# Kernel tuning notes

Hardware: AMD Instinct MI355X
Metric: run time of the kernel (lower is better)

Reference implementation:

```python
import jax, jax.numpy as jnp
import numpy as np

N = 384        # n_res
C = 128        # c_pair
H = 4          # num_head
DH = C // H    # qkv_dim = 32
LN_EPS = 1e-5
NEG_INF = -1e9


def setup_inputs() -> dict:
    key = jax.random.key(0)
    ks = jax.random.split(key, 8)
    s = 0.02
    return {
        "pair": jax.random.normal(ks[0], (N, N, C), dtype=jnp.float32),
        "mask": jax.random.randint(ks[1], (N, N), 0, 2, dtype=jnp.int32),
        "ln_w": jnp.ones((C,), dtype=jnp.float32),
        "ln_b": jnp.zeros((C,), dtype=jnp.float32),
        "w_bias": jax.random.normal(ks[2], (C, H), dtype=jnp.float32) * s,
        "wq": jax.random.normal(ks[3], (C, C), dtype=jnp.float32) * s,
        "wk": jax.random.normal(ks[4], (C, C), dtype=jnp.float32) * s,
        "wv": jax.random.normal(ks[5], (C, C), dtype=jnp.float32) * s,
        "wg": jax.random.normal(ks[6], (C, C), dtype=jnp.float32) * s,
        "wo": jax.random.normal(ks[7], (C, C), dtype=jnp.float32) * s,
    }


def reference(pair, mask, ln_w, ln_b, w_bias, wq, wk, wv, wg, wo):
    # LayerNorm over c_pair (biased variance, as torch)
    mu = pair.mean(-1, keepdims=True)
    var = jnp.mean(jnp.square(pair - mu), axis=-1, keepdims=True)
    x = (pair - mu) * jax.lax.rsqrt(var + LN_EPS) * ln_w + ln_b  # [N,N,C]

    # per-head pair bias: [H, N, N] (query axis q, key axis k)
    bias = jnp.einsum('qkc,ch->hqk', x, w_bias)

    # QKV + gating projections (no bias)
    q = jnp.einsum('bkc,cd->bkd', x, wq).reshape(N, N, H, DH)
    k = jnp.einsum('bkc,cd->bkd', x, wk).reshape(N, N, H, DH)
    v = jnp.einsum('bkc,cd->bkd', x, wv).reshape(N, N, H, DH)

    scale = 1.0 / np.sqrt(DH).astype(np.float32)
    logits = jnp.einsum('bqhd,bkhd->bhqk', q, k) * scale + bias[None]  # [N,H,N,N]
    # mask[b, k]: disallow attending to masked keys in row b
    logits = jnp.where(mask[:, None, None, :] > 0, logits, NEG_INF)
    probs = jax.nn.softmax(logits, axis=-1)

    o = jnp.einsum('bhqk,bkhd->bqhd', probs, v).reshape(N, N, C)
    gate = jax.nn.sigmoid(jnp.einsum('bqc,cd->bqd', x, wg))
    out = jnp.einsum('bqc,cd->bqd', o * gate, wo)  # [N,N,C]
    return out
```

## Files before the change

kernel.cpp:

```cpp
#include <hip/hip_runtime.h>
#include <hip/hip_bf16.h>
#include <stdint.h>

#define NRES 384
#define CPAIR 128
#define NHEAD 4
#define DHEAD 32
#define MROWS (NRES * NRES)
#define QK_SCALE 0.17677669529663687f
#define LOG2E 1.4426950408889634f
#define QK_L2E (0.17677669529663687f * 1.4426950408889634f)

typedef unsigned short u16;
typedef short bf16x8 __attribute__((ext_vector_type(8)));
typedef float f32x4 __attribute__((ext_vector_type(4)));

__device__ __forceinline__ u16 f2bf(float f) {
  union { float f; uint32_t u; } c; c.f = f;
  uint32_t u = c.u + 0x7fff + ((c.u >> 16) & 1);
  return (u16)(u >> 16);
}
__device__ __forceinline__ float bf2f(u16 h) {
  union { uint32_t u; float f; } c; c.u = ((uint32_t)h) << 16; return c.f;
}
__device__ __forceinline__ float fast_exp2(float x) {
#if __has_builtin(__builtin_amdgcn_exp2f)
  return __builtin_amdgcn_exp2f(x);
#else
  return exp2f(x);
#endif
}
__device__ __forceinline__ uint32_t cvt_pk_bf16(float lo, float hi) {
  uint32_t r;
  asm("v_cvt_pk_bf16_f32 %0, %1, %2" : "=v"(r) : "v"(lo), "v"(hi));
  return r;
}

__global__ void prep_kernel(const float* __restrict__ wq, const float* __restrict__ wk,
                            const float* __restrict__ wv, const float* __restrict__ wg,
                            const float* __restrict__ wb, const float* __restrict__ wo,
                            u16* __restrict__ wcat, u16* __restrict__ wot) {
  int tid = blockIdx.x * blockDim.x + threadIdx.x;
  int stride = gridDim.x * blockDim.x;
  for (int i = tid; i < 576 * 128; i += stride) {
    int n = i >> 7, kk = i & 127;
    float val;
    if (n < 128)      val = wq[kk * 128 + n] * QK_L2E;
    else if (n < 256) val = wk[kk * 128 + (n - 128)];
    else if (n < 384) val = wv[kk * 128 + (n - 256)];
    else if (n < 512) val = wg[kk * 128 + (n - 384)];
    else if (n < 516) val = wb[kk * 4 + (n - 512)] * LOG2E;
    else              val = 0.f;
    wcat[i] = f2bf(val);
  }
  for (int i = tid; i < 128 * 128; i += stride) {
    int n = i >> 7, kk = i & 127;
    wot[i] = f2bf(wo[kk * 128 + n]);
  }
}

__global__ __launch_bounds__(256) void proj_kernel(
    const float* __restrict__ pair, const float* __restrict__ lnw,
    const float* __restrict__ lnb, const u16* __restrict__ wcat,
    u16* __restrict__ q, u16* __restrict__ k, u16* __restrict__ v,
    u16* __restrict__ g, float* __restrict__ biasL) {
  __shared__ __align__(16) u16 xs[64 * 136];
  __shared__ __align__(16) u16 wsm[64 * 136];
  const int m0 = blockIdx.x * 64;
  const int tid = threadIdx.x;
  {
    const int row = tid >> 2, q4 = tid & 3;
    const float* pr = pair + (size_t)(m0 + row) * CPAIR + q4 * 32;
    float4 vals[8];
    float s1 = 0.f, s2 = 0.f;
#pragma unroll
    for (int i = 0; i < 8; ++i) {
      vals[i] = ((const float4*)pr)[i];
      s1 += (vals[i].x + vals[i].y) + (vals[i].z + vals[i].w);
      s2 += vals[i].x * vals[i].x + vals[i].y * vals[i].y +
            vals[i].z * vals[i].z + vals[i].w * vals[i].w;
    }
    s1 += __shfl_xor(s1, 1); s1 += __shfl_xor(s1, 2);
    s2 += __shfl_xor(s2, 1); s2 += __shfl_xor(s2, 2);
    const float mu = s1 * (1.f / 128.f);
    const float rs = rsqrtf(s2 * (1.f / 128.f) - mu * mu + 1e-5f);
    const float* wr = lnw + q4 * 32;
    const float* br = lnb + q4 * 32;
    uint32_t packed[16];
#pragma unroll
    for (int i = 0; i < 8; ++i) {
      float4 w4 = ((const float4*)wr)[i];
      float4 b4 = ((const float4*)br)[i];
      float y0 = (vals[i].x - mu) * rs * w4.x + b4.x;
      float y1 = (vals[i].y - mu) * rs * w4.y + b4.y;
      float y2 = (vals[i].z - mu) * rs * w4.z + b4.z;
      float y3 = (vals[i].w - mu) * rs * w4.w + b4.w;
      packed[i * 2]     = (uint32_t)f2bf(y0) | ((uint32_t)f2bf(y1) << 16);
      packed[i * 2 + 1] = (uint32_t)f2bf(y2) | ((uint32_t)f2bf(y3) << 16);
    }
#pragma unroll
    for (int i = 0; i < 4; ++i)
      *(uint4*)&xs[row * 136 + q4 * 32 + i * 8] = *(uint4*)&packed[i * 4];
  }
  const int w = tid >> 6, lane = tid & 63, lm = lane & 15, quad = lane >> 4;
  const int srow = tid >> 4, scol8 = (tid & 15) * 8;

  {
    uint4 st[4];
#pragma unroll
    for (int i = 0; i < 4; ++i)
      st[i] = *(const uint4*)&wcat[(size_t)(srow + i * 16) * CPAIR + scol8];
#pragma unroll
    for (int i = 0; i < 4; ++i)
      *(uint4*)&wsm[(srow + i * 16) * 136 + scol8] = st[i];
  }
  __syncthreads();

  for (int nc = 0; nc < 9; ++nc) {
    if (nc > 0) __syncthreads();
    f32x4 acc[4] = {{0, 0, 0, 0}, {0, 0, 0, 0}, {0, 0, 0, 0}, {0, 0, 0, 0}};
#pragma unroll
    for (int ks = 0; ks < 4; ++ks) {
      bf16x8 a = *(const bf16x8*)&xs[(w * 16 + lm) * 136 + ks * 32 + quad * 8];
#pragma unroll
      for (int nt = 0; nt < 4; ++nt) {
        if (nc == 8 && nt > 0) continue;
        bf16x8 bb = *(const bf16x8*)&wsm[(nt * 16 + lm) * 136 + ks * 32 + quad * 8];
        acc[nt] = __builtin_amdgcn_mfma_f32_16x16x32_bf16(a, bb, acc[nt], 0, 0, 0);
      }
    }
    __syncthreads();
    const bool pf = (nc + 1) < 9;
    uint4 st[4];
    if (pf) {
#pragma unroll
      for (int i = 0; i < 4; ++i) {
        if ((nc + 1) == 8 && i > 0) break;
        st[i] = *(const uint4*)&wcat[(size_t)((nc + 1) * 64 + srow + i * 16) * CPAIR + scol8];
      }
    }
#pragma unroll
    for (int nt = 0; nt < 4; ++nt) {
      if (nc == 8 && nt > 0) continue;
      int n = nc * 64 + nt * 16 + lm;
#pragma unroll
      for (int r = 0; r < 4; ++r) {
        size_t m = (size_t)(m0 + w * 16 + quad * 4 + r);
        float val = acc[nt][r];
        if (n < 128)      q[m * CPAIR + n] = f2bf(val);
        else if (n < 256) k[m * CPAIR + (n - 128)] = f2bf(val);
        else if (n < 384) v[m * CPAIR + (n - 256)] = f2bf(val);
        else if (n < 512) g[m * CPAIR + (n - 384)] = f2bf(1.f / (1.f + __expf(-val)));
        else if (n < 516) {
          int h = n - 512;
          int q_idx = (int)(m / NRES), k_idx = (int)(m % NRES);
          int qt = q_idx >> 6, l6 = q_idx & 63;
          int ww = l6 >> 4, lmq = l6 & 15;
          int t = k_idx >> 4, qk = (k_idx >> 2) & 3, rk = k_idx & 3;
          size_t idx = ((size_t)((h * 6 + qt) * 24 + t) * 256 +
                        (ww * 64 + qk * 16 + lmq)) * 4 + rk;
          biasL[idx] = val;
        }
      }
    }
    if (pf) {
#pragma unroll
      for (int i = 0; i < 4; ++i) {
        if ((nc + 1) == 8 && i > 0) break;
        *(uint4*)&wsm[(srow + i * 16) * 136 + scol8] = st[i];
      }
    }
  }
}

__global__ __launch_bounds__(512, 4) void attn_kernel(
    const u16* __restrict__ q, const u16* __restrict__ k, const u16* __restrict__ v,
    const u16* __restrict__ g, const float* __restrict__ biasL, const int* __restrict__ mask,
    u16* __restrict__ og) {
  __shared__ __align__(16) u16 Ks[NRES * 40];
  __shared__ __align__(16) u16 Vt[DHEAD * 392];
  __shared__ __align__(16) float mskb[NRES];

  const int b = blockIdx.x, h = blockIdx.y;
  const int tid = threadIdx.x;
  const int w = tid >> 6, lane = tid & 63, lm = lane & 15, quad = lane >> 4;
  const int wv = w & 3, hi = w >> 2;

  const u16* kb = k + (size_t)(b * NRES) * CPAIR + h * DHEAD;
  const u16* vb = v + (size_t)(b * NRES) * CPAIR + h * DHEAD;
  for (int i = tid; i < NRES * 4; i += 512) {
    int kk = i >> 2, c8 = (i & 3) * 8;
    *(uint4*)&Ks[kk * 40 + c8] = *(const uint4*)&kb[(size_t)kk * CPAIR + c8];
  }
  for (int i = tid; i < NRES * 4; i += 512) {
    int d8 = i & 3, kk = i >> 2;
    bf16x8 val = *(const bf16x8*)&vb[(size_t)kk * CPAIR + d8 * 8];
    int G = (kk >> 5) * 4 + ((kk >> 2) & 3);
    int e = (kk & 3) + 4 * ((kk >> 4) & 1);
    int col = (((G ^ d8) << 3) | e);
#pragma unroll
    for (int j = 0; j < 8; ++j) Vt[(d8 * 8 + j) * 392 + col] = (u16)val[j];
  }
  for (int i = tid; i < NRES; i += 512)
    mskb[i] = (mask[b * NRES + i] > 0) ? 0.f : -4096.f;
  __syncthreads();

  const int f0 = lm >> 3, f1 = (lm + 16) >> 3;

  for (int it = 0; it < 3; ++it) {
    const int qt = hi * 3 + it;
    const int q0 = qt * 64;
    bf16x8 af = *(const bf16x8*)&q[(size_t)(b * NRES + q0 + wv * 16 + lm) * CPAIR +
                                   h * DHEAD + quad * 8];
    const float* bptr = biasL + ((size_t)(h * 6 + qt) * 24) * 1024 + (wv * 64 + lane) * 4;

    float gv0[4], gv1[4];
#pragma unroll
    for (int r = 0; r < 4; ++r) {
      size_t mrow = (size_t)(b * NRES + q0 + wv * 16 + quad * 4 + r);
      gv0[r] = bf2f(g[mrow * CPAIR + h * DHEAD + lm]);
      gv1[r] = bf2f(g[mrow * CPAIR + h * DHEAD + 16 + lm]);
    }

    f32x4 bvp[2][2];
    bvp[0][0] = *(const f32x4*)(bptr + 0 * 1024);
    bvp[0][1] = *(const f32x4*)(bptr + 1 * 1024);
    bvp[1][0] = *(const f32x4*)(bptr + 2 * 1024);
    bvp[1][1] = *(const f32x4*)(bptr + 3 * 1024);

    float rsum = 0.f;
    f32x4 o0 = {0, 0, 0, 0}, o1 = {0, 0, 0, 0};
#pragma unroll
    for (int c = 0; c < 12; ++c) {
      const int t0 = c * 2, t1 = c * 2 + 1;
      f32x4 mq0 = *(const f32x4*)&mskb[t0 * 16 + quad * 4];
      f32x4 mq1 = *(const f32x4*)&mskb[t1 * 16 + quad * 4];
      f32x4 cv0 = bvp[c & 1][0] + mq0;
      f32x4 cv1 = bvp[c & 1][1] + mq1;
      if (c < 10) {
        bvp[c & 1][0] = *(const f32x4*)(bptr + (t0 + 4) * 1024);
        bvp[c & 1][1] = *(const f32x4*)(bptr + (t1 + 4) * 1024);
      }
      bf16x8 kf0 = *(const bf16x8*)&Ks[(t0 * 16 + lm) * 40 + quad * 8];
      bf16x8 kf1 = *(const bf16x8*)&Ks[(t1 * 16 + lm) * 40 + quad * 8];
      __builtin_amdgcn_s_setprio(1);
      f32x4 s0 = __builtin_amdgcn_mfma_f32_16x16x32_bf16(kf0, af, cv0, 0, 0, 0);
      f32x4 s1 = __builtin_amdgcn_mfma_f32_16x16x32_bf16(kf1, af, cv1, 0, 0, 0);
      __builtin_amdgcn_s_setprio(0);
      float p00 = fast_exp2(s0[0]), p01 = fast_exp2(s0[1]);
      float p02 = fast_exp2(s0[2]), p03 = fast_exp2(s0[3]);
      float p10 = fast_exp2(s1[0]), p11 = fast_exp2(s1[1]);
      float p12 = fast_exp2(s1[2]), p13 = fast_exp2(s1[3]);
      rsum += ((p00 + p01) + (p02 + p03)) + ((p10 + p11) + (p12 + p13));
      union { uint32_t u[4]; bf16x8 v8; } pf;
      pf.u[0] = cvt_pk_bf16(p00, p01);
      pf.u[1] = cvt_pk_bf16(p02, p03);
      pf.u[2] = cvt_pk_bf16(p10, p11);
      pf.u[3] = cvt_pk_bf16(p12, p13);
      int B0i = c * 4 + quad;
      bf16x8 vt0 = *(const bf16x8*)&Vt[lm * 392 + ((B0i ^ f0) << 3)];
      bf16x8 vt1 = *(const bf16x8*)&Vt[(lm + 16) * 392 + ((B0i ^ f1) << 3)];
      __builtin_amdgcn_s_setprio(1);
      o0 = __builtin_amdgcn_mfma_f32_16x16x32_bf16(pf.v8, vt0, o0, 0, 0, 0);
      o1 = __builtin_amdgcn_mfma_f32_16x16x32_bf16(pf.v8, vt1, o1, 0, 0, 0);
      __builtin_amdgcn_s_setprio(0);
    }
    rsum += __shfl_xor(rsum, 16);
    rsum += __shfl_xor(rsum, 32);
#pragma unroll
    for (int r = 0; r < 4; ++r) {
      float rall = __shfl(rsum, quad * 4 + r);
      float rinv = 1.f / rall;
      size_t mrow = (size_t)(b * NRES + q0 + wv * 16 + quad * 4 + r);
      int c0 = h * DHEAD + lm, c1 = h * DHEAD + 16 + lm;
      og[mrow * CPAIR + c0] = f2bf(o0[r] * rinv * gv0[r]);
      og[mrow * CPAIR + c1] = f2bf(o1[r] * rinv * gv1[r]);
    }
  }
}

__global__ __launch_bounds__(256) void outproj_kernel(const u16* __restrict__ og,
                                                      const u16* __restrict__ wot,
                                                      float* __restrict__ out) {
  __shared__ __align__(16) u16 xs[64 * 136];
  __shared__ __align__(16) u16 wsm[64 * 136];
  const int m0 = blockIdx.x * 64;
  const int tid = threadIdx.x;
  const int srow = tid >> 4, scol8 = (tid & 15) * 8;
  {
    uint4 xr[4], wr[4];
#pragma unroll
    for (int i = 0; i < 4; ++i)
      xr[i] = *(const uint4*)&og[(size_t)(m0 + srow + i * 16) * CPAIR + scol8];
#pragma unroll
    for (int i = 0; i < 4; ++i)
      wr[i] = *(const uint4*)&wot[(size_t)(srow + i * 16) * CPAIR + scol8];
#pragma unroll
    for (int i = 0; i < 4; ++i)
      *(uint4*)&xs[(srow + i * 16) * 136 + scol8] = xr[i];
#pragma unroll
    for (int i = 0; i < 4; ++i)
      *(uint4*)&wsm[(srow + i * 16) * 136 + scol8] = wr[i];
  }
  __syncthreads();
  const int w = tid >> 6, lane = tid & 63, lm = lane & 15, quad = lane >> 4;
  for (int nc = 0; nc < 2; ++nc) {
    if (nc > 0) __syncthreads();
    f32x4 acc[4] = {{0, 0, 0, 0}, {0, 0, 0, 0}, {0, 0, 0, 0}, {0, 0, 0, 0}};
#pragma unroll
    for (int ks = 0; ks < 4; ++ks) {
      bf16x8 a = *(const bf16x8*)&xs[(w * 16 + lm) * 136 + ks * 32 + quad * 8];
#pragma unroll
      for (int nt = 0; nt < 4; ++nt) {
        bf16x8 bb = *(const bf16x8*)&wsm[(nt * 16 + lm) * 136 + ks * 32 + quad * 8];
        acc[nt] = __builtin_amdgcn_mfma_f32_16x16x32_bf16(a, bb, acc[nt], 0, 0, 0);
      }
    }
    uint4 st[4];
    const bool pf = (nc == 0);
    if (pf) {
      __syncthreads();
#pragma unroll
      for (int i = 0; i < 4; ++i)
        st[i] = *(const uint4*)&wot[(size_t)(64 + srow + i * 16) * CPAIR + scol8];
    }
#pragma unroll
    for (int nt = 0; nt < 4; ++nt) {
      int n = nc * 64 + nt * 16 + lm;
#pragma unroll
      for (int r = 0; r < 4; ++r) {
        size_t m = (size_t)(m0 + w * 16 + quad * 4 + r);
        out[m * CPAIR + n] = acc[nt][r];
      }
    }
    if (pf) {
#pragma unroll
      for (int i = 0; i < 4; ++i)
        *(uint4*)&wsm[(srow + i * 16) * 136 + scol8] = st[i];
    }
  }
}

extern "C" void kernel_launch(void* const* d_in, const int* in_sizes, int n_in,
                              void* d_out, int out_size, void* d_ws, size_t ws_size,
                              hipStream_t stream) {
  const float* pair = (const float*)d_in[0];
  const int* mask = (const int*)d_in[1];
  const float* ln_w = (const float*)d_in[2];
  const float* ln_b = (const float*)d_in[3];
  const float* w_bias = (const float*)d_in[4];
  const float* wq = (const float*)d_in[5];
  const float* wk = (const float*)d_in[6];
  const float* wv = (const float*)d_in[7];
  const float* wg = (const float*)d_in[8];
  const float* wo = (const float*)d_in[9];
  float* out = (float*)d_out;

  u16* qb = (u16*)d_out;
  u16* gb = qb + (size_t)MROWS * CPAIR;

  char* ws = (char*)d_ws;
  const size_t SZ = (size_t)MROWS * CPAIR * 2;
  u16* og = (u16*)(ws);
  u16* kb = (u16*)(ws + SZ);
  u16* vb = (u16*)(ws + 2 * SZ);
  float* biasL = (float*)(ws + 3 * SZ);
  u16* wcat = (u16*)(ws + 3 * SZ + (size_t)NHEAD * MROWS * 4);
  u16* wot = wcat + 576 * 128;

  hipLaunchKernelGGL(prep_kernel, dim3(64), dim3(256), 0, stream,
                     wq, wk, wv, wg, w_bias, wo, wcat, wot);
  hipLaunchKernelGGL(proj_kernel, dim3(MROWS / 64), dim3(256), 0, stream,
                     pair, ln_w, ln_b, wcat, qb, kb, vb, gb, biasL);
  hipLaunchKernelGGL(attn_kernel, dim3(NRES, NHEAD), dim3(512), 0, stream,
                     qb, kb, vb, gb, biasL, mask, og);
  hipLaunchKernelGGL(outproj_kernel, dim3(MROWS / 64), dim3(256), 0, stream,
                     og, wot, out);
}
```

Baseline: 285.1 us.

## Double-buffer weight tiles in proj kernel via direct global-to-LDS loads with XOR swizzle

Weight chunks in the projection kernel now load straight from global memory into a double-buffered shared tile using global_load_lds. The next chunk is prefetched at the top of each iteration so it overlaps the MFMA work and the output stores. Padding is replaced by an XOR column swizzle to avoid bank conflicts, and one barrier per iteration is removed. The cost is extra LDS for the second buffer and reliance on the wave-uniform LDS destination semantics of global_load_lds.

New measurement: 290.0 us. Within noise of the previous version (+1.7%).

```diff
diff --git a/kernel.cpp b/kernel.cpp
--- a/kernel.cpp
+++ b/kernel.cpp
@@ -34,6 +34,11 @@
   uint32_t r;
   asm("v_cvt_pk_bf16_f32 %0, %1, %2" : "=v"(r) : "v"(lo), "v"(hi));
   return r;
+}
+__device__ __forceinline__ void gload_lds16(const u16* g, u16* l) {
+  __builtin_amdgcn_global_load_lds(
+      (const __attribute__((address_space(1))) uint32_t*)g,
+      (__attribute__((address_space(3))) uint32_t*)l, 16, 0, 0);
 }
 
 __global__ void prep_kernel(const float* __restrict__ wq, const float* __restrict__ wk,
@@ -65,7 +70,7 @@
     u16* __restrict__ q, u16* __restrict__ k, u16* __restrict__ v,
     u16* __restrict__ g, float* __restrict__ biasL) {
   __shared__ __align__(16) u16 xs[64 * 136];
-  __shared__ __align__(16) u16 wsm[64 * 136];
+  __shared__ __align__(16) u16 wsm[2][64 * 128];
   const int m0 = blockIdx.x * 64;
   const int tid = threadIdx.x;
   {
@@ -103,21 +108,31 @@
       *(uint4*)&xs[row * 136 + q4 * 32 + i * 8] = *(uint4*)&packed[i * 4];
   }
   const int w = tid >> 6, lane = tid & 63, lm = lane & 15, quad = lane >> 4;
-  const int srow = tid >> 4, scol8 = (tid & 15) * 8;
-
-  {
-    uint4 st[4];
-#pragma unroll
-    for (int i = 0; i < 4; ++i)
-      st[i] = *(const uint4*)&wcat[(size_t)(srow + i * 16) * CPAIR + scol8];
-#pragma unroll
-    for (int i = 0; i < 4; ++i)
-      *(uint4*)&wsm[(srow + i * 16) * 136 + scol8] = st[i];
+  const int w4r = (tid >> 6) * 4;
+  const int prow = tid >> 4;
+  const int pcol0 = (tid & 15) * 8;
+
+#pragma unroll
+  for (int i = 0; i < 4; ++i) {
+    int rl = prow + i * 16;
+    int colg = pcol0 ^ ((rl & 7) * 8);
+    gload_lds16(&wcat[(size_t)rl * CPAIR + colg], &wsm[0][(w4r + i * 16) * CPAIR]);
   }
   __syncthreads();
 
   for (int nc = 0; nc < 9; ++nc) {
-    if (nc > 0) __syncthreads();
+    const int cur = nc & 1;
+    const bool pf = (nc + 1) < 9;
+    if (pf) {
+#pragma unroll
+      for (int i = 0; i < 4; ++i) {
+        if ((nc + 1) == 8 && i > 0) break;
+        int rl = prow + i * 16;
+        int colg = pcol0 ^ ((rl & 7) * 8);
+        gload_lds16(&wcat[(size_t)((nc + 1) * 64 + rl) * CPAIR + colg],
+                    &wsm[cur ^ 1][(w4r + i * 16) * CPAIR]);
+      }
+    }
     f32x4 acc[4] = {{0, 0, 0, 0}, {0, 0, 0, 0}, {0, 0, 0, 0}, {0, 0, 0, 0}};
 #pragma unroll
     for (int ks = 0; ks < 4; ++ks) {
@@ -125,18 +140,9 @@
 #pragma unroll
       for (int nt = 0; nt < 4; ++nt) {
         if (nc == 8 && nt > 0) continue;
-        bf16x8 bb = *(const bf16x8*)&wsm[(nt * 16 + lm) * 136 + ks * 32 + quad * 8];
+        bf16x8 bb = *(const bf16x8*)&wsm[cur][(nt * 16 + lm) * CPAIR +
+                                             ((ks * 32 + quad * 8) ^ ((lm & 7) * 8))];
         acc[nt] = __builtin_amdgcn_mfma_f32_16x16x32_bf16(a, bb, acc[nt], 0, 0, 0);
-      }
-    }
-    __syncthreads();
-    const bool pf = (nc + 1) < 9;
-    uint4 st[4];
-    if (pf) {
-#pragma unroll
-      for (int i = 0; i < 4; ++i) {
-        if ((nc + 1) == 8 && i > 0) break;
-        st[i] = *(const uint4*)&wcat[(size_t)((nc + 1) * 64 + srow + i * 16) * CPAIR + scol8];
       }
     }
 #pragma unroll
@@ -163,13 +169,7 @@
         }
       }
     }
-    if (pf) {
-#pragma unroll
-      for (int i = 0; i < 4; ++i) {
-        if ((nc + 1) == 8 && i > 0) break;
-        *(uint4*)&wsm[(srow + i * 16) * 136 + scol8] = st[i];
-      }
-    }
+    if (pf) __syncthreads();
   }
 }
 
```
